# Kernel optimization log

Hardware: AMD Instinct MI355X
Metric: run time of the kernel (lower is better)

Reference implementation:

```python
import jax, jax.numpy as jnp
import numpy as np

N = 100000   # nodes
E = 1600000  # edges (avg degree 16)
IN = 128
OUT = 64
NEG_SLOPE = 0.01  # nn.LeakyReLU default


def setup_inputs() -> dict:
    key = jax.random.key(0)
    k1, k2, k3, k4 = jax.random.split(key, 4)
    h = jax.random.normal(k1, (N, IN), dtype=jnp.float32)
    edge_src = jax.random.randint(k2, (E,), 0, N, dtype=jnp.int32)
    edge_dst = jax.random.randint(k3, (E,), 0, N, dtype=jnp.int32)
    W = jax.random.normal(k4, (IN, OUT), dtype=jnp.float32) * (1.0 / np.sqrt(IN))
    b = jnp.zeros((OUT,), dtype=jnp.float32)
    return {"h": h, "W": W, "b": b, "edge_src": edge_src, "edge_dst": edge_dst}


def reference(h, W, b, edge_src, edge_dst):
    # DGL GraphConv, norm='both', allow_zero_in_degree=True (degrees clamped to 1)
    ones = jnp.ones((E,), dtype=h.dtype)
    out_deg = jax.ops.segment_sum(ones, edge_src, num_segments=N)
    in_deg = jax.ops.segment_sum(ones, edge_dst, num_segments=N)
    norm_src = jax.lax.rsqrt(jnp.maximum(out_deg, 1.0))  # [N]
    norm_dst = jax.lax.rsqrt(jnp.maximum(in_deg, 1.0))   # [N]
    # in_dim > out_dim: DGL multiplies by W first to shrink edge traffic
    x = (h * norm_src[:, None]) @ W                       # [N, OUT]
    msgs = x[edge_src]                                    # [E, OUT] gather
    agg = jax.ops.segment_sum(msgs, edge_dst, num_segments=N)  # [N, OUT] scatter-add
    rst = agg * norm_dst[:, None] + b
    # LeakyReLU; dropout is identity in eval mode
    return jnp.where(rst >= 0, rst, NEG_SLOPE * rst)
```

## Files before the change

### kernel.cpp

```cpp
#include <hip/hip_runtime.h>

#define IN_DIM 128
#define OUT_DIM 64
#define NEG_SLOPE 0.01f
#define ECHUNK 4096

__device__ inline float bf_lo(unsigned u) { union { unsigned i; float f; } c; c.i = u << 16; return c.f; }
__device__ inline float bf_hi(unsigned u) { union { unsigned i; float f; } c; c.i = u & 0xFFFF0000u; return c.f; }
__device__ inline unsigned short f2b(float f) {
    union { float f; unsigned i; } c; c.f = f;
    unsigned u = c.i + 0x7FFFu + ((c.i >> 16) & 1u);
    return (unsigned short)(u >> 16);
}

__global__ __launch_bounds__(256) void hist_kernel(
    const int* __restrict__ es, const int* __restrict__ ed,
    int* __restrict__ cntA_d, int* __restrict__ cntA_s, int E, int nbuck) {
    __shared__ int hd[512];
    __shared__ int hs[512];
    int t = threadIdx.x;
    for (int i = t; i < nbuck; i += 256) { hd[i] = 0; hs[i] = 0; }
    __syncthreads();
    int base = blockIdx.x * ECHUNK;
    for (int i = t * 4; i < ECHUNK; i += 1024) {
        int e = base + i;
        if (e < E) {
            int4 d4 = *(const int4*)(ed + e);
            int4 s4 = *(const int4*)(es + e);
            atomicAdd(&hd[d4.x >> 8], 1); atomicAdd(&hd[d4.y >> 8], 1);
            atomicAdd(&hd[d4.z >> 8], 1); atomicAdd(&hd[d4.w >> 8], 1);
            atomicAdd(&hs[s4.x >> 8], 1); atomicAdd(&hs[s4.y >> 8], 1);
            atomicAdd(&hs[s4.z >> 8], 1); atomicAdd(&hs[s4.w >> 8], 1);
        }
    }
    __syncthreads();
    int row = blockIdx.x * nbuck;
    for (int i = t; i < nbuck; i += 256) {
        cntA_d[row + i] = hd[i];
        cntA_s[row + i] = hs[i];
    }
}

__global__ __launch_bounds__(512) void cntscan_kernel(
    const int* __restrict__ cntA_d, const int* __restrict__ cntA_s,
    int* __restrict__ cntB_d, int* __restrict__ cntB_s,
    int* __restrict__ tot_d, int* __restrict__ tot_s,
    int nchunk, int nbuck) {
    __shared__ int s[512];
    int t = threadIdx.x;
    int bid = blockIdx.x;
    const int* cntA = (bid < nbuck) ? cntA_d : cntA_s;
    int* cntB = (bid < nbuck) ? cntB_d : cntB_s;
    int* tot = (bid < nbuck) ? tot_d : tot_s;
    int b = (bid < nbuck) ? bid : bid - nbuck;
    int v = (t < nchunk) ? cntA[t * nbuck + b] : 0;
    s[t] = v;
    __syncthreads();
    for (int d = 1; d < 512; d <<= 1) {
        int u = (t >= d) ? s[t - d] : 0;
        __syncthreads();
        s[t] += u;
        __syncthreads();
    }
    if (t < nchunk) cntB[b * nchunk + t] = s[t] - v;
    if (t == 511) tot[b] = s[511];
}

__global__ __launch_bounds__(512) void base_kernel(
    const int* __restrict__ tot_d, const int* __restrict__ tot_s,
    int* __restrict__ base_d, int* __restrict__ base_s, int nbuck) {
    __shared__ int s[512];
    int t = threadIdx.x;
    for (int which = 0; which < 2; ++which) {
        const int* tot = which ? tot_s : tot_d;
        int* base = which ? base_s : base_d;
        int v = (t < nbuck) ? tot[t] : 0;
        s[t] = v;
        __syncthreads();
        for (int d = 1; d < 512; d <<= 1) {
            int u = (t >= d) ? s[t - d] : 0;
            __syncthreads();
            s[t] += u;
            __syncthreads();
        }
        if (t < nbuck) base[t] = s[t] - v;
        if (t == nbuck - 1) base[nbuck] = s[t];
        __syncthreads();
    }
}

__global__ __launch_bounds__(256) void binpack_kernel(
    const int* __restrict__ es, const int* __restrict__ ed,
    const int* __restrict__ base_d, const int* __restrict__ base_s,
    const int* __restrict__ cntB_d, const int* __restrict__ cntB_s,
    int* __restrict__ bp_dst, unsigned char* __restrict__ bp_src,
    int E, int nchunk, int nbuck) {
    __shared__ int ld[512];
    __shared__ int ls[512];
    int t = threadIdx.x;
    int c = blockIdx.x;
    for (int i = t; i < nbuck; i += 256) {
        ld[i] = base_d[i] + cntB_d[i * nchunk + c];
        ls[i] = base_s[i] + cntB_s[i * nchunk + c];
    }
    __syncthreads();
    int base = c * ECHUNK;
    for (int i = t * 4; i < ECHUNK; i += 1024) {
        int e = base + i;
        if (e < E) {
            int4 s4 = *(const int4*)(es + e);
            int4 d4 = *(const int4*)(ed + e);
            int pd, ps;
            pd = atomicAdd(&ld[d4.x >> 8], 1); bp_dst[pd] = s4.x | ((d4.x & 255) << 24);
            pd = atomicAdd(&ld[d4.y >> 8], 1); bp_dst[pd] = s4.y | ((d4.y & 255) << 24);
            pd = atomicAdd(&ld[d4.z >> 8], 1); bp_dst[pd] = s4.z | ((d4.z & 255) << 24);
            pd = atomicAdd(&ld[d4.w >> 8], 1); bp_dst[pd] = s4.w | ((d4.w & 255) << 24);
            ps = atomicAdd(&ls[s4.x >> 8], 1); bp_src[ps] = (unsigned char)(s4.x & 255);
            ps = atomicAdd(&ls[s4.y >> 8], 1); bp_src[ps] = (unsigned char)(s4.y & 255);
            ps = atomicAdd(&ls[s4.z >> 8], 1); bp_src[ps] = (unsigned char)(s4.z & 255);
            ps = atomicAdd(&ls[s4.w >> 8], 1); bp_src[ps] = (unsigned char)(s4.w & 255);
        }
    }
}

__global__ __launch_bounds__(256) void srccount_kernel(
    const unsigned char* __restrict__ bp_src, const int* __restrict__ base_s,
    int* __restrict__ ds, int n) {
    __shared__ int cnt[256];
    int t = threadIdx.x;
    int b = blockIdx.x;
    cnt[t] = 0;
    __syncthreads();
    int lo = base_s[b], hi = base_s[b + 1];
    for (int i = lo + t; i < hi; i += 256) atomicAdd(&cnt[bp_src[i]], 1);
    __syncthreads();
    int node = (b << 8) + t;
    if (node < n) ds[node] = cnt[t];
}

__global__ __launch_bounds__(256) void dstfill_kernel(
    const int* __restrict__ bp_dst, const int* __restrict__ base_d,
    int* __restrict__ off, int* __restrict__ csr, int n, int E) {
    __shared__ int cnt[256];
    __shared__ int s[256];
    __shared__ int cur[256];
    int t = threadIdx.x;
    int b = blockIdx.x;
    cnt[t] = 0;
    __syncthreads();
    int lo = base_d[b], hi = base_d[b + 1];
    for (int i = lo + t; i < hi; i += 256)
        atomicAdd(&cnt[(int)((unsigned)bp_dst[i] >> 24)], 1);
    __syncthreads();
    int v = cnt[t];
    s[t] = v;
    __syncthreads();
    for (int d = 1; d < 256; d <<= 1) {
        int u = (t >= d) ? s[t - d] : 0;
        __syncthreads();
        s[t] += u;
        __syncthreads();
    }
    int obase = lo + s[t] - v;
    int node = (b << 8) + t;
    if (node < n) off[node] = obase;
    cur[t] = obase;
    if (b == 0 && t == 0) off[n] = E;
    __syncthreads();
    for (int i = lo + t; i < hi; i += 256) {
        int w = bp_dst[i];
        int src = w & 0xFFFFFF;
        int d = (int)((unsigned)w >> 24);
        int slot = atomicAdd(&cur[d], 1);
        csr[slot] = src;
    }
}

__global__ __launch_bounds__(256) void gemm_kernel(const float* __restrict__ h,
                                                   const float* __restrict__ W,
                                                   const int* __restrict__ ds,
                                                   unsigned short* __restrict__ x, int n) {
    __shared__ float Ws[IN_DIM * OUT_DIM];
    __shared__ float hs[64][68];
    int tid = threadIdx.x;
    int row0 = blockIdx.x * 64;

    {
        const float4* W4 = (const float4*)W;
        float4* Ws4 = (float4*)Ws;
        for (int i = tid; i < IN_DIM * OUT_DIM / 4; i += 256) Ws4[i] = W4[i];
    }

    int tc = tid & 15, tr = tid >> 4;
    int r0 = tr * 4, c0 = tc * 4;
    float acc[4][4];
#pragma unroll
    for (int i = 0; i < 4; i++)
#pragma unroll
        for (int j = 0; j < 4; j++) acc[i][j] = 0.f;

    for (int kh = 0; kh < 2; ++kh) {
        __syncthreads();
        for (int i = tid; i < 1024; i += 256) {
            int r = i >> 4, kq = i & 15;
            int row = row0 + r;
            float4 v = make_float4(0.f, 0.f, 0.f, 0.f);
            if (row < n) {
                v = ((const float4*)(h + (size_t)row * IN_DIM + kh * 64))[kq];
                float s = rsqrtf((float)max(ds[row], 1));
                v.x *= s; v.y *= s; v.z *= s; v.w *= s;
            }
            *(float4*)&hs[r][kq * 4] = v;
        }
        __syncthreads();
#pragma unroll
        for (int k = 0; k < 64; k += 4) {
            float4 a[4], w[4];
#pragma unroll
            for (int i = 0; i < 4; i++) a[i] = *(const float4*)&hs[r0 + i][k];
            int kg = (kh * 64 + k) * OUT_DIM + c0;
#pragma unroll
            for (int q = 0; q < 4; q++) w[q] = *(const float4*)&Ws[kg + q * OUT_DIM];
#pragma unroll
            for (int q = 0; q < 4; q++) {
#pragma unroll
                for (int i = 0; i < 4; i++) {
                    float aiq = (q == 0) ? a[i].x : (q == 1) ? a[i].y : (q == 2) ? a[i].z : a[i].w;
                    acc[i][0] += aiq * w[q].x;
                    acc[i][1] += aiq * w[q].y;
                    acc[i][2] += aiq * w[q].z;
                    acc[i][3] += aiq * w[q].w;
                }
            }
        }
    }
#pragma unroll
    for (int i = 0; i < 4; i++) {
        int row = row0 + r0 + i;
        if (row < n) {
            unsigned p0 = (unsigned)f2b(acc[i][0]) | ((unsigned)f2b(acc[i][1]) << 16);
            unsigned p1 = (unsigned)f2b(acc[i][2]) | ((unsigned)f2b(acc[i][3]) << 16);
            uint2 pk = make_uint2(p0, p1);
            *(uint2*)&x[(size_t)row * OUT_DIM + c0] = pk;
        }
    }
}

__global__ __launch_bounds__(256) void gather_kernel(const unsigned short* __restrict__ x,
                                                     const int* __restrict__ csr,
                                                     const int* __restrict__ off,
                                                     const float* __restrict__ b,
                                                     float* __restrict__ out, int n) {
    int g = threadIdx.x >> 3;
    int p = threadIdx.x & 7;
    int v = blockIdx.x * 32 + g;
    if (v >= n) return;
    int s0 = off[v], s1 = off[v + 1];
    float a0 = 0.f, a1 = 0.f, a2 = 0.f, a3 = 0.f, a4 = 0.f, a5 = 0.f, a6 = 0.f, a7 = 0.f;
    int j = s0;
    for (; j + 2 <= s1; j += 2) {
        int n0 = csr[j], n1 = csr[j + 1];
        uint4 w0 = ((const uint4*)(x + (size_t)n0 * OUT_DIM))[p];
        uint4 w1 = ((const uint4*)(x + (size_t)n1 * OUT_DIM))[p];
        a0 += bf_lo(w0.x) + bf_lo(w1.x);
        a1 += bf_hi(w0.x) + bf_hi(w1.x);
        a2 += bf_lo(w0.y) + bf_lo(w1.y);
        a3 += bf_hi(w0.y) + bf_hi(w1.y);
        a4 += bf_lo(w0.z) + bf_lo(w1.z);
        a5 += bf_hi(w0.z) + bf_hi(w1.z);
        a6 += bf_lo(w0.w) + bf_lo(w1.w);
        a7 += bf_hi(w0.w) + bf_hi(w1.w);
    }
    if (j < s1) {
        uint4 w0 = ((const uint4*)(x + (size_t)csr[j] * OUT_DIM))[p];
        a0 += bf_lo(w0.x); a1 += bf_hi(w0.x);
        a2 += bf_lo(w0.y); a3 += bf_hi(w0.y);
        a4 += bf_lo(w0.z); a5 += bf_hi(w0.z);
        a6 += bf_lo(w0.w); a7 += bf_hi(w0.w);
    }
    float nd = rsqrtf((float)max(s1 - s0, 1));
    float4 b0 = ((const float4*)b)[p * 2];
    float4 b1 = ((const float4*)b)[p * 2 + 1];
    float4 r0, r1;
    r0.x = a0 * nd + b0.x; r0.y = a1 * nd + b0.y;
    r0.z = a2 * nd + b0.z; r0.w = a3 * nd + b0.w;
    r1.x = a4 * nd + b1.x; r1.y = a5 * nd + b1.y;
    r1.z = a6 * nd + b1.z; r1.w = a7 * nd + b1.w;
    r0.x = (r0.x >= 0.f) ? r0.x : NEG_SLOPE * r0.x;
    r0.y = (r0.y >= 0.f) ? r0.y : NEG_SLOPE * r0.y;
    r0.z = (r0.z >= 0.f) ? r0.z : NEG_SLOPE * r0.z;
    r0.w = (r0.w >= 0.f) ? r0.w : NEG_SLOPE * r0.w;
    r1.x = (r1.x >= 0.f) ? r1.x : NEG_SLOPE * r1.x;
    r1.y = (r1.y >= 0.f) ? r1.y : NEG_SLOPE * r1.y;
    r1.z = (r1.z >= 0.f) ? r1.z : NEG_SLOPE * r1.z;
    r1.w = (r1.w >= 0.f) ? r1.w : NEG_SLOPE * r1.w;
    float* orow = out + (size_t)v * OUT_DIM + p * 8;
    *(float4*)orow = r0;
    *(float4*)(orow + 4) = r1;
}

extern "C" void kernel_launch(void* const* d_in, const int* in_sizes, int n_in,
                              void* d_out, int out_size, void* d_ws, size_t ws_size,
                              hipStream_t stream) {
    const float* h = (const float*)d_in[0];
    const float* W = (const float*)d_in[1];
    const float* b = (const float*)d_in[2];
    const int* esrc = (const int*)d_in[3];
    const int* edst = (const int*)d_in[4];
    int n = in_sizes[0] / IN_DIM;
    int E = in_sizes[3];
    float* out = (float*)d_out;

    char* ws = (char*)d_ws;
    int* ds  = (int*)ws;
    int* off = (int*)(ws + (size_t)n * 4);
    int* csr = (int*)(ws + (size_t)n * 8 + 16);
    unsigned short* x = (unsigned short*)(ws + (size_t)n * 8 + 16 + (size_t)E * 4);

    int nchunk = (E + ECHUNK - 1) / ECHUNK;
    int nbuck  = (n + 255) >> 8;

    char* xb = (char*)x;
    int* bp_dst = (int*)xb;
    unsigned char* bp_src = (unsigned char*)(xb + 6600000);
    int* cntA_d = (int*)(xb + 8400000);
    int* cntA_s = (int*)(xb + 9100000);
    int* cntB_d = (int*)(xb + 9800000);
    int* cntB_s = (int*)(xb + 10500000);
    int* tot_d  = (int*)(xb + 11200000);
    int* tot_s  = (int*)(xb + 11210000);
    int* base_d = (int*)(xb + 11220000);
    int* base_s = (int*)(xb + 11230000);

    hist_kernel<<<nchunk, 256, 0, stream>>>(esrc, edst, cntA_d, cntA_s, E, nbuck);
    cntscan_kernel<<<2 * nbuck, 512, 0, stream>>>(cntA_d, cntA_s, cntB_d, cntB_s,
                                                  tot_d, tot_s, nchunk, nbuck);
    base_kernel<<<1, 512, 0, stream>>>(tot_d, tot_s, base_d, base_s, nbuck);
    binpack_kernel<<<nchunk, 256, 0, stream>>>(esrc, edst, base_d, base_s,
                                               cntB_d, cntB_s, bp_dst, bp_src,
                                               E, nchunk, nbuck);
    srccount_kernel<<<nbuck, 256, 0, stream>>>(bp_src, base_s, ds, n);
    dstfill_kernel<<<nbuck, 256, 0, stream>>>(bp_dst, base_d, off, csr, n, E);
    gemm_kernel<<<(n + 63) / 64, 256, 0, stream>>>(h, W, ds, x, n);
    gather_kernel<<<(n + 31) / 32, 256, 0, stream>>>(x, csr, off, b, out, n);
}
```

Before: 151.1 us.

## Use bf16 MFMA for node GEMM and unroll gather loop by four

```diff
diff --git a/kernel.cpp b/kernel.cpp
--- a/kernel.cpp
+++ b/kernel.cpp
@@ -4,6 +4,9 @@
 #define OUT_DIM 64
 #define NEG_SLOPE 0.01f
 #define ECHUNK 4096
+
+typedef __attribute__((ext_vector_type(8))) short short8;
+typedef __attribute__((ext_vector_type(4))) float floatx4;
 
 __device__ inline float bf_lo(unsigned u) { union { unsigned i; float f; } c; c.i = u << 16; return c.f; }
 __device__ inline float bf_hi(unsigned u) { union { unsigned i; float f; } c; c.i = u & 0xFFFF0000u; return c.f; }
@@ -180,68 +183,71 @@
                                                    const float* __restrict__ W,
                                                    const int* __restrict__ ds,
                                                    unsigned short* __restrict__ x, int n) {
-    __shared__ float Ws[IN_DIM * OUT_DIM];
-    __shared__ float hs[64][68];
+    __shared__ unsigned short Wt[OUT_DIM][136];
     int tid = threadIdx.x;
-    int row0 = blockIdx.x * 64;
 
     {
         const float4* W4 = (const float4*)W;
-        float4* Ws4 = (float4*)Ws;
-        for (int i = tid; i < IN_DIM * OUT_DIM / 4; i += 256) Ws4[i] = W4[i];
-    }
-
-    int tc = tid & 15, tr = tid >> 4;
-    int r0 = tr * 4, c0 = tc * 4;
-    float acc[4][4];
-#pragma unroll
-    for (int i = 0; i < 4; i++)
-#pragma unroll
-        for (int j = 0; j < 4; j++) acc[i][j] = 0.f;
-
-    for (int kh = 0; kh < 2; ++kh) {
-        __syncthreads();
-        for (int i = tid; i < 1024; i += 256) {
-            int r = i >> 4, kq = i & 15;
-            int row = row0 + r;
-            float4 v = make_float4(0.f, 0.f, 0.f, 0.f);
-            if (row < n) {
-                v = ((const float4*)(h + (size_t)row * IN_DIM + kh * 64))[kq];
-                float s = rsqrtf((float)max(ds[row], 1));
-                v.x *= s; v.y *= s; v.z *= s; v.w *= s;
-            }
-            *(float4*)&hs[r][kq * 4] = v;
-        }
-        __syncthreads();
-#pragma unroll
-        for (int k = 0; k < 64; k += 4) {
-            float4 a[4], w[4];
-#pragma unroll
-            for (int i = 0; i < 4; i++) a[i] = *(const float4*)&hs[r0 + i][k];
-            int kg = (kh * 64 + k) * OUT_DIM + c0;
-#pragma unroll
-            for (int q = 0; q < 4; q++) w[q] = *(const float4*)&Ws[kg + q * OUT_DIM];
-#pragma unroll
-            for (int q = 0; q < 4; q++) {
-#pragma unroll
-                for (int i = 0; i < 4; i++) {
-                    float aiq = (q == 0) ? a[i].x : (q == 1) ? a[i].y : (q == 2) ? a[i].z : a[i].w;
-                    acc[i][0] += aiq * w[q].x;
-                    acc[i][1] += aiq * w[q].y;
-                    acc[i][2] += aiq * w[q].z;
-                    acc[i][3] += aiq * w[q].w;
-                }
-            }
-        }
-    }
-#pragma unroll
-    for (int i = 0; i < 4; i++) {
-        int row = row0 + r0 + i;
-        if (row < n) {
-            unsigned p0 = (unsigned)f2b(acc[i][0]) | ((unsigned)f2b(acc[i][1]) << 16);
-            unsigned p1 = (unsigned)f2b(acc[i][2]) | ((unsigned)f2b(acc[i][3]) << 16);
-            uint2 pk = make_uint2(p0, p1);
-            *(uint2*)&x[(size_t)row * OUT_DIM + c0] = pk;
+        for (int i = tid; i < IN_DIM * OUT_DIM / 4; i += 256) {
+            float4 v = W4[i];
+            int k = i >> 4, c = (i & 15) * 4;
+            Wt[c + 0][k] = f2b(v.x);
+            Wt[c + 1][k] = f2b(v.y);
+            Wt[c + 2][k] = f2b(v.z);
+            Wt[c + 3][k] = f2b(v.w);
+        }
+    }
+    __syncthreads();
+
+    int wid = tid >> 6, lane = tid & 63;
+    int rbase = blockIdx.x * 64 + wid * 16;
+    int row = rbase + (lane & 15);
+    int kg = lane >> 4;
+    int rowc = min(row, n - 1);
+
+    const float* hrow = h + (size_t)rowc * IN_DIM + kg * 8;
+    float4 af[8];
+#pragma unroll
+    for (int ks = 0; ks < 4; ks++) {
+        af[2 * ks]     = *(const float4*)(hrow + ks * 32);
+        af[2 * ks + 1] = *(const float4*)(hrow + ks * 32 + 4);
+    }
+    short8 afr[4];
+#pragma unroll
+    for (int ks = 0; ks < 4; ks++) {
+        afr[ks][0] = (short)f2b(af[2 * ks].x);
+        afr[ks][1] = (short)f2b(af[2 * ks].y);
+        afr[ks][2] = (short)f2b(af[2 * ks].z);
+        afr[ks][3] = (short)f2b(af[2 * ks].w);
+        afr[ks][4] = (short)f2b(af[2 * ks + 1].x);
+        afr[ks][5] = (short)f2b(af[2 * ks + 1].y);
+        afr[ks][6] = (short)f2b(af[2 * ks + 1].z);
+        afr[ks][7] = (short)f2b(af[2 * ks + 1].w);
+    }
+
+    floatx4 acc[4];
+#pragma unroll
+    for (int gf = 0; gf < 4; gf++) acc[gf] = (floatx4){0.f, 0.f, 0.f, 0.f};
+
+#pragma unroll
+    for (int ks = 0; ks < 4; ks++) {
+#pragma unroll
+        for (int gf = 0; gf < 4; gf++) {
+            int col = gf * 16 + (lane & 15);
+            short8 bfr = *(const short8*)&Wt[col][ks * 32 + kg * 8];
+            acc[gf] = __builtin_amdgcn_mfma_f32_16x16x32_bf16(afr[ks], bfr, acc[gf], 0, 0, 0);
+        }
+    }
+
+#pragma unroll
+    for (int r = 0; r < 4; r++) {
+        int orow = rbase + (lane >> 4) * 4 + r;
+        if (orow < n) {
+            float sc = rsqrtf((float)max(ds[orow], 1));
+            unsigned short* xr = x + (size_t)orow * OUT_DIM + (lane & 15);
+#pragma unroll
+            for (int gf = 0; gf < 4; gf++)
+                xr[gf * 16] = f2b(acc[gf][r] * sc);
         }
     }
 }
@@ -258,20 +264,22 @@
     int s0 = off[v], s1 = off[v + 1];
     float a0 = 0.f, a1 = 0.f, a2 = 0.f, a3 = 0.f, a4 = 0.f, a5 = 0.f, a6 = 0.f, a7 = 0.f;
     int j = s0;
-    for (; j + 2 <= s1; j += 2) {
-        int n0 = csr[j], n1 = csr[j + 1];
+    for (; j + 4 <= s1; j += 4) {
+        int n0 = csr[j], n1 = csr[j + 1], n2 = csr[j + 2], n3 = csr[j + 3];
         uint4 w0 = ((const uint4*)(x + (size_t)n0 * OUT_DIM))[p];
         uint4 w1 = ((const uint4*)(x + (size_t)n1 * OUT_DIM))[p];
-        a0 += bf_lo(w0.x) + bf_lo(w1.x);
-        a1 += bf_hi(w0.x) + bf_hi(w1.x);
-        a2 += bf_lo(w0.y) + bf_lo(w1.y);
-        a3 += bf_hi(w0.y) + bf_hi(w1.y);
-        a4 += bf_lo(w0.z) + bf_lo(w1.z);
-        a5 += bf_hi(w0.z) + bf_hi(w1.z);
-        a6 += bf_lo(w0.w) + bf_lo(w1.w);
-        a7 += bf_hi(w0.w) + bf_hi(w1.w);
-    }
-    if (j < s1) {
+        uint4 w2 = ((const uint4*)(x + (size_t)n2 * OUT_DIM))[p];
+        uint4 w3 = ((const uint4*)(x + (size_t)n3 * OUT_DIM))[p];
+        a0 += (bf_lo(w0.x) + bf_lo(w1.x)) + (bf_lo(w2.x) + bf_lo(w3.x));
+        a1 += (bf_hi(w0.x) + bf_hi(w1.x)) + (bf_hi(w2.x) + bf_hi(w3.x));
+        a2 += (bf_lo(w0.y) + bf_lo(w1.y)) + (bf_lo(w2.y) + bf_lo(w3.y));
+        a3 += (bf_hi(w0.y) + bf_hi(w1.y)) + (bf_hi(w2.y) + bf_hi(w3.y));
+        a4 += (bf_lo(w0.z) + bf_lo(w1.z)) + (bf_lo(w2.z) + bf_lo(w3.z));
+        a5 += (bf_hi(w0.z) + bf_hi(w1.z)) + (bf_hi(w2.z) + bf_hi(w3.z));
+        a6 += (bf_lo(w0.w) + bf_lo(w1.w)) + (bf_lo(w2.w) + bf_lo(w3.w));
+        a7 += (bf_hi(w0.w) + bf_hi(w1.w)) + (bf_hi(w2.w) + bf_hi(w3.w));
+    }
+    for (; j < s1; j++) {
         uint4 w0 = ((const uint4*)(x + (size_t)csr[j] * OUT_DIM))[p];
         a0 += bf_lo(w0.x); a1 += bf_hi(w0.x);
         a2 += bf_lo(w0.y); a3 += bf_hi(w0.y);
```

Measured after the change: 134.1 us. 1.13x faster.
